# Kernel optimization log

Measured on AMD Instinct MI355X. Metric: run time of the kernel, lower is better.

The kernel has to match this reference:

```python
import jax, jax.numpy as jnp
import numpy as np

D_MODEL = 2048
NUM_HEADS = 16
HEAD_DIM = D_MODEL // NUM_HEADS
BATCH = 4
SEQ = 2048


def setup_inputs() -> dict:
    key = jax.random.key(0)
    ks = jax.random.split(key, 9)
    s = 1.0 / np.sqrt(D_MODEL)  # mimic reasonable init scale
    return {
        "x": jax.random.normal(ks[0], (BATCH, SEQ, D_MODEL), dtype=jnp.float32),
        "Wq": jax.random.normal(ks[1], (D_MODEL, D_MODEL), dtype=jnp.float32) * s,
        "bq": jnp.zeros((D_MODEL,), dtype=jnp.float32),
        "Wk": jax.random.normal(ks[2], (D_MODEL, D_MODEL), dtype=jnp.float32) * s,
        "bk": jnp.zeros((D_MODEL,), dtype=jnp.float32),
        "Wv": jax.random.normal(ks[3], (D_MODEL, D_MODEL), dtype=jnp.float32) * s,
        "bv": jnp.zeros((D_MODEL,), dtype=jnp.float32),
        "Wo": jax.random.normal(ks[4], (D_MODEL, D_MODEL), dtype=jnp.float32) * s,
        "bo": jnp.zeros((D_MODEL,), dtype=jnp.float32),
    }


def _split_heads(t):
    b, s, _ = t.shape
    return t.reshape(b, s, NUM_HEADS, HEAD_DIM).transpose(0, 2, 1, 3)  # [b,h,s,d]


def reference(x, Wq, bq, Wk, bk, Wv, bv, Wo, bo):
    # Projections (torch Linear: y = x @ W^T + b; here W stored as [in, out] so x @ W + b)
    q = _split_heads(x @ Wq + bq)
    k = _split_heads(x @ Wk + bk)
    v = _split_heads(x @ Wv + bv)

    scale = 1.0 / np.sqrt(HEAD_DIM)
    scores = jnp.einsum("bhqd,bhkd->bhqk", q, k) * scale  # [b,h,s,s]
    s = x.shape[1]
    causal = jnp.tril(jnp.ones((s, s), dtype=bool))
    scores = jnp.where(causal[None, None], scores, jnp.float32(-jnp.inf))
    attn = jax.nn.softmax(scores, axis=-1)
    out = jnp.einsum("bhqk,bhkd->bhqd", attn, v)
    out = out.transpose(0, 2, 1, 3).reshape(x.shape[0], s, D_MODEL)  # merge heads
    return out @ Wo + bo
```

## Files before the change

### kernel.cpp

```cpp
#include <hip/hip_runtime.h>
#include <hip/hip_bf16.h>
#include <math.h>

#define SEQ   2048
#define DM    2048
#define NH    16
#define HD    128
#define MROWS 8192

typedef __bf16 bf16x8 __attribute__((ext_vector_type(8)));
typedef __bf16 bf16x4 __attribute__((ext_vector_type(4)));
typedef float  f32x4  __attribute__((ext_vector_type(4)));

#define MFMA16(a, b, c) __builtin_amdgcn_mfma_f32_16x16x32_bf16((a), (b), (c), 0, 0, 0)

__device__ __forceinline__ void g2l16(const void* g, void* l) {
    __builtin_amdgcn_global_load_lds(
        (const __attribute__((address_space(1))) void*)g,
        (__attribute__((address_space(3))) void*)l, 16, 0, 0);
}

#define SFENCE() asm volatile("" ::: "memory")
#define BARRIER() do { SFENCE(); __builtin_amdgcn_s_barrier(); SFENCE(); } while (0)

__global__ void prep_fused(const float* __restrict__ x,
                           const float* __restrict__ s0,
                           const float* __restrict__ s1,
                           const float* __restrict__ s2,
                           const float* __restrict__ s3,
                           __bf16* __restrict__ xb,
                           __bf16* __restrict__ wdst) {
    const int bx = blockIdx.x;
    if (bx < 16384) {
        __shared__ float t[32][33];
        const int z = bx >> 12, rem = bx & 4095;
        const float* src = (z == 0) ? s0 : (z == 1) ? s1 : (z == 2) ? s2 : s3;
        __bf16* d = wdst + (size_t)z * DM * DM;
        const int c0 = (rem & 63) * 32, r0 = (rem >> 6) * 32;
        for (int i = threadIdx.y; i < 32; i += 8)
            t[i][threadIdx.x] = src[(size_t)(r0 + i) * DM + c0 + threadIdx.x];
        __syncthreads();
        for (int i = threadIdx.y; i < 32; i += 8)
            d[(size_t)(c0 + i) * DM + r0 + threadIdx.x] = (__bf16)t[threadIdx.x][i];
    } else {
        const int tid = threadIdx.y * 32 + threadIdx.x;
        const size_t i0 = (((size_t)(bx - 16384)) * 256 + tid) * 8;
        if (i0 + 8 <= (size_t)MROWS * DM) {
            f32x4 a = *(const f32x4*)(x + i0);
            f32x4 b = *(const f32x4*)(x + i0 + 4);
            bf16x8 o;
#pragma unroll
            for (int j = 0; j < 4; ++j) { o[j] = (__bf16)a[j]; o[4 + j] = (__bf16)b[j]; }
            *(bf16x8*)(xb + i0) = o;
        }
    }
}

template <int MODE>
__global__ __launch_bounds__(512, 2) void gemm_bt(const __bf16* __restrict__ A,
                                                  const __bf16* __restrict__ Bt,
                                                  const float* __restrict__ b0,
                                                  const float* __restrict__ b1,
                                                  const float* __restrict__ b2,
                                                  void* __restrict__ Cout_,
                                                  __bf16* __restrict__ Vt_) {
    constexpr int K  = DM;
    constexpr int NT = K / 64;
    __shared__ __align__(16) __bf16 smem[65536];
    const int tid  = threadIdx.x;
    const int wave = tid >> 6, lane = tid & 63;
    const int quad = lane >> 4, l16 = lane & 15;
    const int wm = (wave >> 2) * 128, wn = (wave & 3) * 64;

    const int nwgx = gridDim.x;
    const int nwg  = nwgx * gridDim.y;
    const int wg   = blockIdx.y * nwgx + blockIdx.x;
    const int swzb = (wg & 7) * (nwg >> 3) + (wg >> 3);
    const int bm = (swzb % nwgx) * 256;
    const int bn = (swzb / nwgx) * 256;

    const int proj = (MODE == 0) ? (bn >> 11) : 0;
    const float* bias = (MODE == 0) ? (proj == 0 ? b0 : (proj == 1 ? b1 : b2)) : b0;

    const int r8   = lane >> 3;
    const int cSrc = (lane & 7) ^ r8;
    const __bf16* aSrc = A  + (size_t)(bm + wave * 8 + r8) * K + cSrc * 8;
    const __bf16* bSrc = Bt + (size_t)(bn + wave * 8 + r8) * K + cSrc * 8;
    const int ldsW = wave * 8 * 64;

    __bf16* As0 = smem;          __bf16* Bs0 = smem + 16384;
    __bf16* As1 = smem + 32768;  __bf16* Bs1 = smem + 49152;

    auto stage = [&](const __bf16* srcLane, __bf16* dstTile, int half, int t) {
#pragma unroll
        for (int q = 0; q < 2; ++q) {
            const int rr = half * 128 + q * 64;
            g2l16(srcLane + (size_t)rr * K + t * 64, dstTile + rr * 64 + ldsW);
        }
    };

    f32x4 acc[8][4];
#pragma unroll
    for (int i = 0; i < 8; ++i)
#pragma unroll
        for (int j = 0; j < 4; ++j) acc[i][j] = (f32x4){0.f, 0.f, 0.f, 0.f};

    stage(bSrc, Bs0, 0, 0);
    stage(aSrc, As0, 0, 0);
    stage(bSrc, Bs0, 1, 0);
    stage(aSrc, As0, 1, 0);
    if (NT > 1) { stage(bSrc, Bs1, 0, 1); stage(aSrc, As1, 0, 1); }
    asm volatile("s_waitcnt vmcnt(4)" ::: "memory");
    BARRIER();

    const int swz8 = l16 & 7;
    bf16x8 ah[4][2], bh[4][2];

    for (int t = 0; t < NT; ++t) {
        __bf16* As  = (t & 1) ? As1 : As0;
        __bf16* Bs  = (t & 1) ? Bs1 : Bs0;
        __bf16* Asn = (t & 1) ? As0 : As1;
        __bf16* Bsn = (t & 1) ? Bs0 : Bs1;

#pragma unroll
        for (int i = 0; i < 4; ++i)
#pragma unroll
            for (int kk = 0; kk < 2; ++kk)
                ah[i][kk] = *(const bf16x8*)(As + (wm + i * 16 + l16) * 64 +
                                             (((kk * 4 + quad) ^ swz8) * 8));
#pragma unroll
        for (int j = 0; j < 2; ++j)
#pragma unroll
            for (int kk = 0; kk < 2; ++kk)
                bh[j][kk] = *(const bf16x8*)(Bs + (wn + j * 16 + l16) * 64 +
                                             (((kk * 4 + quad) ^ swz8) * 8));
        if (t + 1 < NT) stage(bSrc, Bsn, 1, t + 1);
        BARRIER();
        __builtin_amdgcn_s_setprio(1);
#pragma unroll
        for (int i = 0; i < 4; ++i)
#pragma unroll
            for (int j = 0; j < 2; ++j) {
                acc[i][j] = MFMA16(ah[i][0], bh[j][0], acc[i][j]);
                acc[i][j] = MFMA16(ah[i][1], bh[j][1], acc[i][j]);
            }
        __builtin_amdgcn_s_setprio(0);
        BARRIER();

#pragma unroll
        for (int j = 2; j < 4; ++j)
#pragma unroll
            for (int kk = 0; kk < 2; ++kk)
                bh[j][kk] = *(const bf16x8*)(Bs + (wn + j * 16 + l16) * 64 +
                                             (((kk * 4 + quad) ^ swz8) * 8));
        if (t + 1 < NT) stage(aSrc, Asn, 1, t + 1);
        BARRIER();
        __builtin_amdgcn_s_setprio(1);
#pragma unroll
        for (int i = 0; i < 4; ++i)
#pragma unroll
            for (int j = 2; j < 4; ++j) {
                acc[i][j] = MFMA16(ah[i][0], bh[j][0], acc[i][j]);
                acc[i][j] = MFMA16(ah[i][1], bh[j][1], acc[i][j]);
            }
        __builtin_amdgcn_s_setprio(0);
        BARRIER();

#pragma unroll
        for (int i = 0; i < 4; ++i)
#pragma unroll
            for (int kk = 0; kk < 2; ++kk)
                ah[i][kk] = *(const bf16x8*)(As + (wm + 64 + i * 16 + l16) * 64 +
                                             (((kk * 4 + quad) ^ swz8) * 8));
        if (t + 2 < NT) stage(bSrc, Bs, 0, t + 2);
        BARRIER();
        __builtin_amdgcn_s_setprio(1);
#pragma unroll
        for (int i = 0; i < 4; ++i)
#pragma unroll
            for (int j = 0; j < 2; ++j) {
                acc[4 + i][j] = MFMA16(ah[i][0], bh[j][0], acc[4 + i][j]);
                acc[4 + i][j] = MFMA16(ah[i][1], bh[j][1], acc[4 + i][j]);
            }
        __builtin_amdgcn_s_setprio(0);
        BARRIER();

        if (t + 2 < NT) stage(aSrc, As, 0, t + 2);
        BARRIER();
        __builtin_amdgcn_s_setprio(1);
#pragma unroll
        for (int i = 0; i < 4; ++i)
#pragma unroll
            for (int j = 2; j < 4; ++j) {
                acc[4 + i][j] = MFMA16(ah[i][0], bh[j][0], acc[4 + i][j]);
                acc[4 + i][j] = MFMA16(ah[i][1], bh[j][1], acc[4 + i][j]);
            }
        __builtin_amdgcn_s_setprio(0);
        if (t + 2 < NT) asm volatile("s_waitcnt vmcnt(4)" ::: "memory");
        else            asm volatile("s_waitcnt vmcnt(0)" ::: "memory");
        BARRIER();
    }

    if (MODE == 0 && proj == 2) {
        __bf16* wb = smem + wave * 4608;
        const int b_ = bm >> 11;
        const int p8 = lane >> 3, c8 = lane & 7;
#pragma unroll
        for (int ih = 0; ih < 2; ++ih) {
#pragma unroll
            for (int j = 0; j < 4; ++j) {
                const int n = (bn + wn + j * 16 + l16) & (DM - 1);
                const float bia = bias[n];
#pragma unroll
                for (int ii = 0; ii < 4; ++ii) {
                    bf16x4 pk;
#pragma unroll
                    for (int r = 0; r < 4; ++r)
                        pk[r] = (__bf16)(acc[ih * 4 + ii][j][r] + bia);
                    *(bf16x4*)(wb + (j * 16 + l16) * 72 + ii * 16 + quad * 4) = pk;
                }
            }
#pragma unroll
            for (int p = 0; p < 8; ++p) {
                const int d_loc = p * 8 + p8;
                const int n = (bn + wn + d_loc) & (DM - 1);
                const int h = n >> 7, d = n & (HD - 1);
                bf16x8 v = *(const bf16x8*)(wb + d_loc * 72 + c8 * 8);
                const int s = (bm & (SEQ - 1)) + wm + ih * 64 + c8 * 8;
                *(bf16x8*)(Vt_ + ((size_t)((b_ * NH + h) * HD + d)) * SEQ + s) = v;
            }
        }
        return;
    }

    if (MODE == 0) {
        __bf16* out = (__bf16*)Cout_ + (size_t)proj * MROWS * DM;
#pragma unroll
        for (int i = 0; i < 8; ++i) {
            const int m = bm + wm + i * 16 + quad * 4;
            const int b_ = m >> 11, s0 = m & (SEQ - 1);
#pragma unroll
            for (int j = 0; j < 4; ++j) {
                const int n = (bn + wn + j * 16 + l16) & (DM - 1);
                const int h = n >> 7, d = n & (HD - 1);
                const float bia = bias[n];
#pragma unroll
                for (int r = 0; r < 4; ++r)
                    out[((size_t)((b_ * NH + h) * SEQ + s0 + r)) * HD + d] =
                        (__bf16)(acc[i][j][r] + bia);
            }
        }
    } else {
        float* out = (float*)Cout_;
#pragma unroll
        for (int i = 0; i < 8; ++i) {
            const int m = bm + wm + i * 16 + quad * 4;
#pragma unroll
            for (int j = 0; j < 4; ++j) {
                const int n = bn + wn + j * 16 + l16;
                const float bia = bias[n];
#pragma unroll
                for (int r = 0; r < 4; ++r)
                    out[(size_t)(m + r) * DM + n] = acc[i][j][r] + bia;
            }
        }
    }
}

__global__ __launch_bounds__(512) void fa_fwd(const __bf16* __restrict__ Q,
                                              const __bf16* __restrict__ Kg,
                                              const __bf16* __restrict__ Vt,
                                              __bf16* __restrict__ O) {
    __shared__ __bf16 Ks[64 * 128];
    __shared__ __bf16 Vs[128 * 64];
    __shared__ __bf16 Pt[8][16 * 72];
    const int tid  = threadIdx.x;
    const int wave = tid >> 6, lane = tid & 63;
    const int quad = lane >> 4, l16 = lane & 15;
    const int bh = blockIdx.y;
    const int bx = gridDim.x - 1 - blockIdx.x;
    const int q0 = bx * 128;
    const int qrow0 = q0 + wave * 16;
    __bf16* Pw = &Pt[wave][0];

    auto stageK = [&](int k0s) {
#pragma unroll
        for (int j = 0; j < 2; ++j) {
            const int reg  = wave * 2 + j;
            const int rowK = reg * 4 + (lane >> 4);
            const int cK   = (lane & 15) ^ (rowK & 7);
            g2l16(Kg + (size_t)(bh * SEQ + k0s + rowK) * HD + cK * 8, Ks + reg * 512);
        }
    };
    auto stageV = [&](int k0s) {
#pragma unroll
        for (int j = 0; j < 2; ++j) {
            const int reg  = wave * 2 + j;
            const int rowV = reg * 8 + (lane >> 3);
            const int cV   = (lane & 7) ^ (rowV & 7);
            g2l16(Vt + (size_t)(bh * HD + rowV) * SEQ + k0s + cV * 8, Vs + reg * 512);
        }
    };

    bf16x8 qf[4];
    const __bf16* qrow = Q + (size_t)(bh * SEQ + qrow0 + l16) * HD;
#pragma unroll
    for (int kc = 0; kc < 4; ++kc) qf[kc] = *(const bf16x8*)(qrow + kc * 32 + quad * 8);

    float m_q = -INFINITY, l_q = 0.f;
    f32x4 oacc[8];
#pragma unroll
    for (int ot = 0; ot < 8; ++ot) oacc[ot] = (f32x4){0.f, 0.f, 0.f, 0.f};

    const float sl2 = 0.08838834764831845f * 1.4426950408889634f;

    stageK(0);
    stageV(0);
    asm volatile("s_waitcnt vmcnt(2)" ::: "memory");
    BARRIER();

    const int ntiles = bx * 2 + 2;
    for (int kt = 0; kt < ntiles; ++kt) {
        const int k0 = kt * 64;
        const bool work = (k0 <= qrow0 + 15);
        const int swz = l16 & 7;
        f32x4 st[4];

        if (work) {
            __builtin_amdgcn_s_setprio(1);
#pragma unroll
            for (int t = 0; t < 4; ++t) {
                f32x4 a = (f32x4){0.f, 0.f, 0.f, 0.f};
#pragma unroll
                for (int kc = 0; kc < 4; ++kc) {
                    bf16x8 kf = *(const bf16x8*)(Ks + (t * 16 + l16) * 128 +
                                                 (((kc * 4 + quad) ^ swz) * 8));
                    a = MFMA16(kf, qf[kc], a);
                }
#pragma unroll
                for (int r = 0; r < 4; ++r) st[t][r] = a[r] * sl2;
            }
            __builtin_amdgcn_s_setprio(0);
        }
        asm volatile("s_waitcnt lgkmcnt(0)" ::: "memory");
        BARRIER();
        if (kt + 1 < ntiles) stageK(k0 + 64);

        if (work) {
            if (kt >= ntiles - 2) {
                const int q = qrow0 + l16;
#pragma unroll
                for (int t = 0; t < 4; ++t)
#pragma unroll
                    for (int r = 0; r < 4; ++r) {
                        const int key = k0 + t * 16 + quad * 4 + r;
                        if (key > q) st[t][r] = -INFINITY;
                    }
            }
            float vm = st[0][0];
#pragma unroll
            for (int t = 0; t < 4; ++t)
#pragma unroll
                for (int r = 0; r < 4; ++r) vm = fmaxf(vm, st[t][r]);
            vm = fmaxf(vm, __shfl_xor(vm, 16));
            vm = fmaxf(vm, __shfl_xor(vm, 32));
            const float mn = fmaxf(m_q, vm);
            const float alpha = __builtin_amdgcn_exp2f(m_q - mn);
            m_q = mn;
            float ps = 0.f;
#pragma unroll
            for (int t = 0; t < 4; ++t)
#pragma unroll
                for (int r = 0; r < 4; ++r) {
                    const float p = __builtin_amdgcn_exp2f(st[t][r] - mn);
                    st[t][r] = p;
                    ps += p;
                }
            ps += __shfl_xor(ps, 16);
            ps += __shfl_xor(ps, 32);
            l_q = l_q * alpha + ps;
#pragma unroll
            for (int ot = 0; ot < 8; ++ot)
#pragma unroll
                for (int r = 0; r < 4; ++r) oacc[ot][r] *= alpha;

#pragma unroll
            for (int t = 0; t < 4; ++t) {
                bf16x4 pk;
#pragma unroll
                for (int r = 0; r < 4; ++r) pk[r] = (__bf16)st[t][r];
                *(bf16x4*)(Pw + l16 * 72 + t * 16 + quad * 4) = pk;
            }
        }
        if (kt + 1 < ntiles) asm volatile("s_waitcnt vmcnt(2)" ::: "memory");
        else                 asm volatile("s_waitcnt vmcnt(0)" ::: "memory");
        BARRIER();

        if (work) {
            __builtin_amdgcn_s_setprio(1);
#pragma unroll
            for (int kk = 0; kk < 2; ++kk) {
                bf16x8 pf = *(const bf16x8*)(Pw + l16 * 72 + kk * 32 + quad * 8);
#pragma unroll
                for (int ot = 0; ot < 8; ++ot) {
                    bf16x8 vf = *(const bf16x8*)(Vs + (ot * 16 + l16) * 64 +
                                                 (((kk * 4 + quad) ^ swz) * 8));
                    oacc[ot] = MFMA16(vf, pf, oacc[ot]);
                }
            }
            __builtin_amdgcn_s_setprio(0);
        }
        asm volatile("s_waitcnt lgkmcnt(0)" ::: "memory");
        BARRIER();
        if (kt + 1 < ntiles) {
            stageV(k0 + 64);
            asm volatile("s_waitcnt vmcnt(2)" ::: "memory");
        }
        BARRIER();
    }

    const int b = bh >> 4, h = bh & (NH - 1);
    const float inv = 1.0f / l_q;
    __bf16* orow = O + ((size_t)(b * SEQ + qrow0 + l16)) * DM + h * HD;
#pragma unroll
    for (int ot = 0; ot < 8; ++ot) {
        bf16x4 ov;
#pragma unroll
        for (int r = 0; r < 4; ++r) ov[r] = (__bf16)(oacc[ot][r] * inv);
        *(bf16x4*)(orow + ot * 16 + quad * 4) = ov;
    }
}

extern "C" void kernel_launch(void* const* d_in, const int* in_sizes, int n_in,
                              void* d_out, int out_size, void* d_ws, size_t ws_size,
                              hipStream_t stream) {
    (void)in_sizes; (void)n_in; (void)out_size; (void)ws_size;
    const float* x  = (const float*)d_in[0];
    const float* Wq = (const float*)d_in[1];
    const float* bq = (const float*)d_in[2];
    const float* Wk = (const float*)d_in[3];
    const float* bk = (const float*)d_in[4];
    const float* Wv = (const float*)d_in[5];
    const float* bv = (const float*)d_in[6];
    const float* Wo = (const float*)d_in[7];
    const float* bo = (const float*)d_in[8];

    char* ws = (char*)d_ws;
    const size_t WT = (size_t)DM * DM * 2;
    const size_t XB = (size_t)MROWS * DM * 2;
    __bf16* WTs = (__bf16*)ws;
    __bf16* WoT = (__bf16*)(ws + 3 * WT);
    __bf16* xb  = (__bf16*)(ws + 4 * WT + 0 * XB);
    __bf16* Qb  = (__bf16*)(ws + 4 * WT + 1 * XB);
    __bf16* Kb  = (__bf16*)(ws + 4 * WT + 2 * XB);
    __bf16* Vtb = (__bf16*)(ws + 4 * WT + 3 * XB);
    __bf16* Ob  = xb;

    const dim3 tb(32, 8);
    prep_fused<<<16384 + 8192, tb, 0, stream>>>(x, Wq, Wk, Wv, Wo, xb, WTs);

    gemm_bt<0><<<dim3(32, 24), 512, 0, stream>>>(xb, WTs, bq, bk, bv, Qb, Vtb);

    fa_fwd<<<dim3(SEQ / 128, 4 * NH), 512, 0, stream>>>(Qb, Kb, Vtb, Ob);

    gemm_bt<1><<<dim3(32, 8), 512, 0, stream>>>(Ob, WoT, bo, nullptr, nullptr,
                                                (float*)d_out, nullptr);
}
```

Before: 605.1 us.

## Process 32 query rows per wave in flash attention to reuse K/V tiles

New measurement: 646.0 us. 1.07x slower.

```diff
diff --git a/kernel.cpp b/kernel.cpp
--- a/kernel.cpp
+++ b/kernel.cpp
@@ -267,10 +267,10 @@
     }
 }
 
-__global__ __launch_bounds__(512) void fa_fwd(const __bf16* __restrict__ Q,
-                                              const __bf16* __restrict__ Kg,
-                                              const __bf16* __restrict__ Vt,
-                                              __bf16* __restrict__ O) {
+__global__ __launch_bounds__(512, 2) void fa_fwd(const __bf16* __restrict__ Q,
+                                                 const __bf16* __restrict__ Kg,
+                                                 const __bf16* __restrict__ Vt,
+                                                 __bf16* __restrict__ O) {
     __shared__ __bf16 Ks[64 * 128];
     __shared__ __bf16 Vs[128 * 64];
     __shared__ __bf16 Pt[8][16 * 72];
@@ -279,8 +279,8 @@
     const int quad = lane >> 4, l16 = lane & 15;
     const int bh = blockIdx.y;
     const int bx = gridDim.x - 1 - blockIdx.x;
-    const int q0 = bx * 128;
-    const int qrow0 = q0 + wave * 16;
+    const int q0 = bx * 256;
+    const int qrow0 = q0 + wave * 32;
     __bf16* Pw = &Pt[wave][0];
 
     auto stageK = [&](int k0s) {
@@ -302,15 +302,21 @@
         }
     };
 
-    bf16x8 qf[4];
-    const __bf16* qrow = Q + (size_t)(bh * SEQ + qrow0 + l16) * HD;
-#pragma unroll
-    for (int kc = 0; kc < 4; ++kc) qf[kc] = *(const bf16x8*)(qrow + kc * 32 + quad * 8);
-
-    float m_q = -INFINITY, l_q = 0.f;
-    f32x4 oacc[8];
-#pragma unroll
-    for (int ot = 0; ot < 8; ++ot) oacc[ot] = (f32x4){0.f, 0.f, 0.f, 0.f};
+    bf16x8 qf[2][4];
+#pragma unroll
+    for (int cb = 0; cb < 2; ++cb) {
+        const __bf16* qrow = Q + (size_t)(bh * SEQ + qrow0 + cb * 16 + l16) * HD;
+#pragma unroll
+        for (int kc = 0; kc < 4; ++kc)
+            qf[cb][kc] = *(const bf16x8*)(qrow + kc * 32 + quad * 8);
+    }
+
+    float m_q[2] = {-INFINITY, -INFINITY}, l_q[2] = {0.f, 0.f};
+    f32x4 oacc[2][8];
+#pragma unroll
+    for (int cb = 0; cb < 2; ++cb)
+#pragma unroll
+        for (int ot = 0; ot < 8; ++ot) oacc[cb][ot] = (f32x4){0.f, 0.f, 0.f, 0.f};
 
     const float sl2 = 0.08838834764831845f * 1.4426950408889634f;
 
@@ -319,26 +325,30 @@
     asm volatile("s_waitcnt vmcnt(2)" ::: "memory");
     BARRIER();
 
-    const int ntiles = bx * 2 + 2;
+    const int ntiles = bx * 4 + 4;
+    const int swz = l16 & 7;
     for (int kt = 0; kt < ntiles; ++kt) {
         const int k0 = kt * 64;
-        const bool work = (k0 <= qrow0 + 15);
-        const int swz = l16 & 7;
-        f32x4 st[4];
+        const bool work  = (k0 <= qrow0);
+        const bool maskt = (k0 + 64 > qrow0);
+        f32x4 st[2][4];
 
         if (work) {
             __builtin_amdgcn_s_setprio(1);
 #pragma unroll
             for (int t = 0; t < 4; ++t) {
-                f32x4 a = (f32x4){0.f, 0.f, 0.f, 0.f};
+                f32x4 a0 = (f32x4){0.f, 0.f, 0.f, 0.f};
+                f32x4 a1 = (f32x4){0.f, 0.f, 0.f, 0.f};
 #pragma unroll
                 for (int kc = 0; kc < 4; ++kc) {
                     bf16x8 kf = *(const bf16x8*)(Ks + (t * 16 + l16) * 128 +
                                                  (((kc * 4 + quad) ^ swz) * 8));
-                    a = MFMA16(kf, qf[kc], a);
+                    a0 = MFMA16(kf, qf[0][kc], a0);
+                    a1 = MFMA16(kf, qf[1][kc], a1);
                 }
 #pragma unroll
-                for (int r = 0; r < 4; ++r) st[t][r] = a[r] * sl2;
+                for (int r = 0; r < 4; ++r) { st[0][t][r] = a0[r] * sl2;
+                                              st[1][t][r] = a1[r] * sl2; }
             }
             __builtin_amdgcn_s_setprio(0);
         }
@@ -347,49 +357,47 @@
         if (kt + 1 < ntiles) stageK(k0 + 64);
 
         if (work) {
-            if (kt >= ntiles - 2) {
-                const int q = qrow0 + l16;
+            if (maskt) {
+#pragma unroll
+                for (int cb = 0; cb < 2; ++cb) {
+                    const int q = qrow0 + cb * 16 + l16;
+#pragma unroll
+                    for (int t = 0; t < 4; ++t)
+#pragma unroll
+                        for (int r = 0; r < 4; ++r) {
+                            const int key = k0 + t * 16 + quad * 4 + r;
+                            if (key > q) st[cb][t][r] = -INFINITY;
+                        }
+                }
+            }
+#pragma unroll
+            for (int cb = 0; cb < 2; ++cb) {
+                float vm = st[cb][0][0];
 #pragma unroll
                 for (int t = 0; t < 4; ++t)
 #pragma unroll
+                    for (int r = 0; r < 4; ++r) vm = fmaxf(vm, st[cb][t][r]);
+                vm = fmaxf(vm, __shfl_xor(vm, 16));
+                vm = fmaxf(vm, __shfl_xor(vm, 32));
+                const float mn = fmaxf(m_q[cb], vm);
+                const float alpha = __builtin_amdgcn_exp2f(m_q[cb] - mn);
+                m_q[cb] = mn;
+                float ps = 0.f;
+#pragma unroll
+                for (int t = 0; t < 4; ++t)
+#pragma unroll
                     for (int r = 0; r < 4; ++r) {
-                        const int key = k0 + t * 16 + quad * 4 + r;
-                        if (key > q) st[t][r] = -INFINITY;
+                        const float p = __builtin_amdgcn_exp2f(st[cb][t][r] - mn);
+                        st[cb][t][r] = p;
+                        ps += p;
                     }
-            }
-            float vm = st[0][0];
-#pragma unroll
-            for (int t = 0; t < 4; ++t)
-#pragma unroll
-                for (int r = 0; r < 4; ++r) vm = fmaxf(vm, st[t][r]);
-            vm = fmaxf(vm, __shfl_xor(vm, 16));
-            vm = fmaxf(vm, __shfl_xor(vm, 32));
-            const float mn = fmaxf(m_q, vm);
-            const float alpha = __builtin_amdgcn_exp2f(m_q - mn);
-            m_q = mn;
-            float ps = 0.f;
-#pragma unroll
-            for (int t = 0; t < 4; ++t)
-#pragma unroll
-                for (int r = 0; r < 4; ++r) {
-                    const float p = __builtin_amdgcn_exp2f(st[t][r] - mn);
-                    st[t][r] = p;
-                    ps += p;
-                }
-            ps += __shfl_xor(ps, 16);
-            ps += __shfl_xor(ps, 32);
-            l_q = l_q * alpha + ps;
-#pragma unroll
-            for (int ot = 0; ot < 8; ++ot)
-#pragma unroll
-                for (int r = 0; r < 4; ++r) oacc[ot][r] *= alpha;
-
-#pragma unroll
-            for (int t = 0; t < 4; ++t) {
-                bf16x4 pk;
-#pragma unroll
-                for (int r = 0; r < 4; ++r) pk[r] = (__bf16)st[t][r];
-                *(bf16x4*)(Pw + l16 * 72 + t * 16 + quad * 4) = pk;
+                ps += __shfl_xor(ps, 16);
+                ps += __shfl_xor(ps, 32);
+                l_q[cb] = l_q[cb] * alpha + ps;
+#pragma unroll
+                for (int ot = 0; ot < 8; ++ot)
+#pragma unroll
+                    for (int r = 0; r < 4; ++r) oacc[cb][ot][r] *= alpha;
             }
         }
         if (kt + 1 < ntiles) asm volatile("s_waitcnt vmcnt(2)" ::: "memory");
@@ -397,17 +405,30 @@
         BARRIER();
 
         if (work) {
+            bf16x8 pf[2][2];
+#pragma unroll
+            for (int cb = 0; cb < 2; ++cb) {
+#pragma unroll
+                for (int t = 0; t < 4; ++t) {
+                    bf16x4 pk;
+#pragma unroll
+                    for (int r = 0; r < 4; ++r) pk[r] = (__bf16)st[cb][t][r];
+                    *(bf16x4*)(Pw + l16 * 72 + t * 16 + quad * 4) = pk;
+                }
+#pragma unroll
+                for (int kk = 0; kk < 2; ++kk)
+                    pf[cb][kk] = *(const bf16x8*)(Pw + l16 * 72 + kk * 32 + quad * 8);
+            }
             __builtin_amdgcn_s_setprio(1);
 #pragma unroll
-            for (int kk = 0; kk < 2; ++kk) {
-                bf16x8 pf = *(const bf16x8*)(Pw + l16 * 72 + kk * 32 + quad * 8);
+            for (int kk = 0; kk < 2; ++kk)
 #pragma unroll
                 for (int ot = 0; ot < 8; ++ot) {
                     bf16x8 vf = *(const bf16x8*)(Vs + (ot * 16 + l16) * 64 +
                                                  (((kk * 4 + quad) ^ swz) * 8));
-                    oacc[ot] = MFMA16(vf, pf, oacc[ot]);
+                    oacc[0][ot] = MFMA16(vf, pf[0][kk], oacc[0][ot]);
+                    oacc[1][ot] = MFMA16(vf, pf[1][kk], oacc[1][ot]);
                 }
-            }
             __builtin_amdgcn_s_setprio(0);
         }
         asm volatile("s_waitcnt lgkmcnt(0)" ::: "memory");
@@ -420,14 +441,17 @@
     }
 
     const int b = bh >> 4, h = bh & (NH - 1);
-    const float inv = 1.0f / l_q;
-    __bf16* orow = O + ((size_t)(b * SEQ + qrow0 + l16)) * DM + h * HD;
-#pragma unroll
-    for (int ot = 0; ot < 8; ++ot) {
-        bf16x4 ov;
-#pragma unroll
-        for (int r = 0; r < 4; ++r) ov[r] = (__bf16)(oacc[ot][r] * inv);
-        *(bf16x4*)(orow + ot * 16 + quad * 4) = ov;
+#pragma unroll
+    for (int cb = 0; cb < 2; ++cb) {
+        const float inv = 1.0f / l_q[cb];
+        __bf16* orow = O + ((size_t)(b * SEQ + qrow0 + cb * 16 + l16)) * DM + h * HD;
+#pragma unroll
+        for (int ot = 0; ot < 8; ++ot) {
+            bf16x4 ov;
+#pragma unroll
+            for (int r = 0; r < 4; ++r) ov[r] = (__bf16)(oacc[cb][ot][r] * inv);
+            *(bf16x4*)(orow + ot * 16 + quad * 4) = ov;
+        }
     }
 }
 
@@ -461,7 +485,7 @@
 
     gemm_bt<0><<<dim3(32, 24), 512, 0, stream>>>(xb, WTs, bq, bk, bv, Qb, Vtb);
 
-    fa_fwd<<<dim3(SEQ / 128, 4 * NH), 512, 0, stream>>>(Qb, Kb, Vtb, Ob);
+    fa_fwd<<<dim3(SEQ / 256, 4 * NH), 512, 0, stream>>>(Qb, Kb, Vtb, Ob);
 
     gemm_bt<1><<<dim3(32, 8), 512, 0, stream>>>(Ob, WoT, bo, nullptr, nullptr,
                                                 (float*)d_out, nullptr);
```
